# Optimization experiments

Hardware: AMD Instinct MI355X
Metric: run time of the kernel (lower is better)

## Reference

```python
import jax, jax.numpy as jnp
import numpy as np

GROUPS = 2048   # number of FPS centroids S
K = 24          # ball-query neighbors
RADIUS = 0.2    # ball radius (xyz in unit cube)


def setup_inputs() -> dict:
    key = jax.random.key(0)
    k1, k2 = jax.random.split(key)
    xyz = jax.random.uniform(k1, (8, 8192, 3), dtype=jnp.float32)
    points = jax.random.normal(k2, (8, 8192, 128), dtype=jnp.float32)
    return {"xyz": xyz, "points": points}


def _fps(xyz, npoint):
    # iterative farthest point sampling; deterministic start at index 0
    B, N, _ = xyz.shape

    def step(carry, _):
        distance, farthest = carry                       # [B,N], [B]
        centroid = jnp.take_along_axis(xyz, farthest[:, None, None], axis=1)  # [B,1,3]
        d = jnp.sum((xyz - centroid) ** 2, axis=-1)      # [B,N]
        distance = jnp.minimum(distance, d)
        nxt = jnp.argmax(distance, axis=-1).astype(jnp.int32)
        return (distance, nxt), farthest

    init = (jnp.full((B, N), 1e10, jnp.float32), jnp.zeros((B,), jnp.int32))
    _, idxs = jax.lax.scan(step, init, None, length=npoint)  # [npoint,B]
    return jnp.transpose(idxs)                               # [B,npoint]


def _index_points(points, idx):
    # points [B,N,C], idx [B,...] -> [B,...,C]
    B = idx.shape[0]
    flat = idx.reshape(B, -1)
    out = jnp.take_along_axis(points, flat[..., None], axis=1)
    return out.reshape(*idx.shape, points.shape[-1])


def _square_distance(src, dst):
    # src [B,N,C], dst [B,M,C] -> [B,N,M]
    return (jnp.sum(src ** 2, -1)[..., None]
            + jnp.sum(dst ** 2, -1)[:, None, :]
            - 2.0 * jnp.einsum('bnc,bmc->bnm', src, dst))


def _query_ball(radius, nsample, xyz, new_xyz):
    B, N, _ = xyz.shape
    sqr = _square_distance(new_xyz, xyz)                 # [B,S,N]
    base = jnp.arange(N, dtype=jnp.int32)
    idx = jnp.where(sqr > radius * radius, jnp.int32(N), base)  # out-of-ball -> N
    idx = jnp.sort(idx, axis=-1)[..., :nsample]          # [B,S,k]
    first = idx[..., :1]
    return jnp.where(idx == N, first, idx)


def reference(xyz, points):
    B, N, _ = xyz.shape
    fps_idx = _fps(xyz, GROUPS)                          # [B,S]
    new_xyz = _index_points(xyz, fps_idx)                # [B,S,3]
    anchor_feat = _index_points(points, fps_idx)         # [B,S,D]
    idx = _query_ball(RADIUS, K, xyz, new_xyz)           # [B,S,k]
    grouped_xyz = _index_points(xyz, idx)                # [B,S,k,3]
    grouped_points = _index_points(points, idx)          # [B,S,k,D]
    grouped = jnp.concatenate([grouped_points, grouped_xyz], axis=-1)  # use_xyz=True
    anchor = jnp.broadcast_to(anchor_feat[:, :, None, :],
                              (B, GROUPS, K, points.shape[-1]))
    new_points = jnp.concatenate([grouped, anchor], axis=-1)  # [B,S,k,2D+3]
    return new_xyz, new_points
```

## Files before the change

kernel.cpp:

```cpp
#include <hip/hip_runtime.h>
#include <stdint.h>


#define NBATCH 8
#define NPTS   8192
#define NCH    128
#define NGROUP 2048
#define NK     24
#define ROWLEN (2 * NCH + 3)

#define FPS_T  512
#define PPT    16

typedef float v2f __attribute__((ext_vector_type(2)));

struct __attribute__((packed, aligned(4))) f4s { float x, y, z, w; };

__device__ __forceinline__ float sq3_nofma(float dx, float dy, float dz) {
#pragma clang fp contract(off)
  return dx * dx + dy * dy + dz * dz;
}

__device__ __forceinline__ float dot3_fma(float ax, float ay, float az,
                                          float bx, float by, float bz) {
  float acc = __fmul_rn(ax, bx);
  acc = __fmaf_rn(ay, by, acc);
  acc = __fmaf_rn(az, bz, acc);
  return acc;
}

__device__ __forceinline__ float ballquery_sqr(float srcSq, float dstSq, float dot) {
#pragma clang fp contract(off)
  return (srcSq + dstSq) - 2.0f * dot;
}

template <int CTRL>
__device__ __forceinline__ float maxdpp(float v) {
  int s = __builtin_amdgcn_update_dpp(__builtin_bit_cast(int, v),
                                      __builtin_bit_cast(int, v),
                                      CTRL, 0xF, 0xF, false);
  return fmaxf(v, __builtin_bit_cast(float, s));
}

__device__ __forceinline__ float readlane_f(float v, int lane) {
  return __builtin_bit_cast(float,
      __builtin_amdgcn_readlane(__builtin_bit_cast(int, v), lane));
}

__global__ __launch_bounds__(FPS_T) void fps_kernel(const float* __restrict__ xyz,
                                                    int* __restrict__ fps_idx) {
  const int b = blockIdx.x;
  const int t = threadIdx.x;
  const int lane = t & 63;
  const int w = t >> 6;
  const float* xb = xyz + (size_t)b * NPTS * 3;

  __shared__ float s_xyz[NPTS * 3];
  union pair_t { struct { float v; int i; }; unsigned long long u; };
  __shared__ __align__(16) pair_t s_p[2][8];

  {
    const float4* src4 = (const float4*)xb;
    float4* dst4 = (float4*)s_xyz;
    for (int i = t; i < (NPTS * 3) / 4; i += FPS_T) dst4[i] = src4[i];
  }

  const int base = t * PPT;
  v2f px[8], py[8], pz[8], d2[8];
#pragma unroll
  for (int j = 0; j < 8; ++j) {
    const int n0 = base + 2 * j;
    px[j].x = xb[n0 * 3 + 0]; py[j].x = xb[n0 * 3 + 1]; pz[j].x = xb[n0 * 3 + 2];
    px[j].y = xb[n0 * 3 + 3]; py[j].y = xb[n0 * 3 + 4]; pz[j].y = xb[n0 * 3 + 5];
    d2[j].x = 1e10f; d2[j].y = 1e10f;
  }

  float cx = xb[0], cy = xb[1], cz = xb[2];
  if (t == 0) fps_idx[b * NGROUP + 0] = 0;

  for (int s = 1; s < NGROUP; ++s) {
    const int p = s & 1;

    float lv = -1.0f;
#pragma unroll
    for (int j = 0; j < 8; ++j) {
      v2f dx, dy, dz, dd, nd;
      {
#pragma clang fp contract(off)
        dx = px[j] - cx;
        dy = py[j] - cy;
        dz = pz[j] - cz;
        dd = dx * dx + dy * dy + dz * dz;
      }
      nd.x = fminf(d2[j].x, dd.x);
      nd.y = fminf(d2[j].y, dd.y);
      d2[j] = nd;
      lv = fmaxf(fmaxf(nd.x, nd.y), lv);
    }
    int kk = 0;
#pragma unroll
    for (int j = 7; j >= 0; --j) {
      if (d2[j].y == lv) kk = 2 * j + 1;
      if (d2[j].x == lv) kk = 2 * j;
    }
    const int li = base + kk;

    float v = lv;
    v = maxdpp<0x111>(v);
    v = maxdpp<0x112>(v);
    v = maxdpp<0x114>(v);
    v = maxdpp<0x118>(v);
    v = maxdpp<0x142>(v);
    v = maxdpp<0x143>(v);
    const float wmax = readlane_f(v, 63);
    const unsigned long long m = __ballot(lv == wmax);
    const int wl = (int)__builtin_ctzll(m);
    const int wli = __builtin_amdgcn_readlane(li, wl);
    if (lane == 0) {
      s_p[p][w].u = ((unsigned long long)(unsigned)wli << 32) |
                    (unsigned long long)__builtin_bit_cast(unsigned, wmax);
    }
    __syncthreads();

    const float4* q = (const float4*)&s_p[p][0];
    const float4 q0 = q[0], q1 = q[1], q2 = q[2], q3 = q[3];
    float bv = q0.x;
    float biF = q0.y;
    {
      const float vv[7] = { q0.z, q1.x, q1.z, q2.x, q2.z, q3.x, q3.z };
      const float ii[7] = { q0.w, q1.y, q1.w, q2.y, q2.w, q3.y, q3.w };
#pragma unroll
      for (int k = 0; k < 7; ++k) {
        const bool gt = vv[k] > bv;
        bv  = gt ? vv[k] : bv;
        biF = gt ? ii[k] : biF;
      }
    }
    const int bi = __builtin_bit_cast(int, biF);

    if (t == 0) fps_idx[b * NGROUP + s] = bi;

    const int b3 = bi * 3;
    cx = s_xyz[b3 + 0];
    cy = s_xyz[b3 + 1];
    cz = s_xyz[b3 + 2];
  }
}

__global__ __launch_bounds__(256) void group_kernel(const float* __restrict__ xyz,
                                                    const float* __restrict__ points,
                                                    const int* __restrict__ fps_idx,
                                                    float* __restrict__ out) {
  const int bx = blockIdx.x;
  const int gb = ((bx & 7) << 11) | (bx >> 3);
  const int b = gb >> 11;
  const int tid = threadIdx.x;
  const float* xb = xyz + (size_t)b * NPTS * 3;
  const float* pb = points + (size_t)b * NPTS * NCH;

  __shared__ int s_idx[NK];

  const int a_idx = fps_idx[gb];
  const float cx = xb[a_idx * 3 + 0];
  const float cy = xb[a_idx * 3 + 1];
  const float cz = xb[a_idx * 3 + 2];
  const float srcSq = sq3_nofma(cx, cy, cz);
  const float R2 = (float)(0.2 * 0.2);

  if (tid < 64) {
    int cnt = 0;
    int first = 0;
    const unsigned long long below = ((unsigned long long)1 << tid) - 1ull;
    for (int chunk = 0; chunk < NPTS / 128; ++chunk) {
      const int n0 = (chunk << 7) + (tid << 1);
      const float* p = xb + (size_t)n0 * 3;
      const float2 A = *(const float2*)(p + 0);
      const float2 Bv = *(const float2*)(p + 2);
      const float2 C = *(const float2*)(p + 4);
      const float x0 = A.x, y0 = A.y, z0 = Bv.x;
      const float x1 = Bv.y, y1 = C.x, z1 = C.y;

      const float sqr0 = ballquery_sqr(srcSq, sq3_nofma(x0, y0, z0),
                                       dot3_fma(cx, cy, cz, x0, y0, z0));
      const float sqr1 = ballquery_sqr(srcSq, sq3_nofma(x1, y1, z1),
                                       dot3_fma(cx, cy, cz, x1, y1, z1));
      const bool ok0 = !(sqr0 > R2);
      const bool ok1 = !(sqr1 > R2);
      const unsigned long long m0 = __ballot(ok0);
      const unsigned long long m1 = __ballot(ok1);
      if (cnt == 0 && (m0 | m1)) {
        const int f0 = m0 ? (int)__builtin_ctzll(m0) : 64;
        const int f1 = m1 ? (int)__builtin_ctzll(m1) : 64;
        first = (f0 <= f1) ? ((chunk << 7) + 2 * f0) : ((chunk << 7) + 2 * f1 + 1);
      }
      const int p0 = cnt + (int)__popcll(m0 & below) + (int)__popcll(m1 & below);
      const int p1 = p0 + (ok0 ? 1 : 0);
      if (ok0 && p0 < NK) s_idx[p0] = n0;
      if (ok1 && p1 < NK) s_idx[p1] = n0 + 1;
      cnt += (int)__popcll(m0) + (int)__popcll(m1);
      if (cnt >= NK) break;
    }
    if (tid >= cnt && tid < NK) s_idx[tid] = first;
  }
  __syncthreads();

  if (tid == 0) {
    float* onx = out + (size_t)gb * 3;
    onx[0] = cx; onx[1] = cy; onx[2] = cz;
  }

  float* op = out + (size_t)NBATCH * NGROUP * 3 + (size_t)gb * (NK * ROWLEN);
  const float* anchor = pb + (size_t)a_idx * NCH;

#pragma unroll
  for (int it = 0; it < 3; ++it) {
    const int vidx = tid + (it << 8);
    const int k = vidx >> 5;
    const int c4 = vidx & 31;
    const int si = s_idx[k];
    const f4s val = *(const f4s*)(pb + (size_t)si * NCH + (c4 << 2));
    *(f4s*)(op + k * ROWLEN + (c4 << 2)) = val;
  }
#pragma unroll
  for (int it = 0; it < 3; ++it) {
    const int vidx = tid + (it << 8);
    const int k = vidx >> 5;
    const int c4 = vidx & 31;
    const f4s val = *(const f4s*)(anchor + (c4 << 2));
    *(f4s*)(op + k * ROWLEN + (NCH + 3) + (c4 << 2)) = val;
  }
  if (tid < NK * 3) {
    const int k = tid / 3;
    const int r = tid - k * 3;
    const int si = s_idx[k];
    op[k * ROWLEN + NCH + r] = xb[si * 3 + r];
  }
}

extern "C" void kernel_launch(void* const* d_in, const int* in_sizes, int n_in,
                              void* d_out, int out_size, void* d_ws, size_t ws_size,
                              hipStream_t stream) {
  const float* xyz = (const float*)d_in[0];
  const float* points = (const float*)d_in[1];
  float* out = (float*)d_out;
  int* fps_idx = (int*)d_ws;

  fps_kernel<<<dim3(NBATCH), dim3(FPS_T), 0, stream>>>(xyz, fps_idx);
  group_kernel<<<dim3(NBATCH * NGROUP), dim3(256), 0, stream>>>(xyz, points, fps_idx, out);
}
```

Baseline: 2.134 ms.

## Fuse FPS and grouping into one persistent kernel with flag-based streaming

Merges the sequential FPS kernel and the grouping kernel into one launch. Eight blocks run FPS and publish each centroid index with atomic stores, while 248 persistent consumer blocks spin on a -1-initialised workspace and perform ball query and gather as soon as each index appears. The aim is to hide the grouping and gather work behind the long serial FPS loop. It adds a memset, spin-waiting, and a deadlock risk if the FPS blocks are not all co-resident with the consumers, and the consumer blocks may contend for resources with the FPS blocks.

```diff
diff --git a/kernel.cpp b/kernel.cpp
--- a/kernel.cpp
+++ b/kernel.cpp
@@ -9,8 +9,11 @@
 #define NK     24
 #define ROWLEN (2 * NCH + 3)
 
-#define FPS_T  512
-#define PPT    16
+#define FPS_T   512
+#define PPT     16
+#define GBLOCKS 248
+#define GSLOTS  62
+#define GITERS  34
 
 typedef float v2f __attribute__((ext_vector_type(2)));
 
@@ -47,193 +50,221 @@
       __builtin_amdgcn_readlane(__builtin_bit_cast(int, v), lane));
 }
 
-__global__ __launch_bounds__(FPS_T) void fps_kernel(const float* __restrict__ xyz,
-                                                    int* __restrict__ fps_idx) {
-  const int b = blockIdx.x;
+__global__ __launch_bounds__(FPS_T) void fused_kernel(const float* __restrict__ xyz,
+                                                      const float* __restrict__ points,
+                                                      int* __restrict__ fps_idx,
+                                                      float* __restrict__ out) {
   const int t = threadIdx.x;
-  const int lane = t & 63;
-  const int w = t >> 6;
-  const float* xb = xyz + (size_t)b * NPTS * 3;
 
   __shared__ float s_xyz[NPTS * 3];
   union pair_t { struct { float v; int i; }; unsigned long long u; };
   __shared__ __align__(16) pair_t s_p[2][8];
-
-  {
-    const float4* src4 = (const float4*)xb;
-    float4* dst4 = (float4*)s_xyz;
-    for (int i = t; i < (NPTS * 3) / 4; i += FPS_T) dst4[i] = src4[i];
+  __shared__ int s_aidx[2];
+  __shared__ int s_idx2[2][NK];
+
+  if (blockIdx.x < NBATCH) {
+    const int b = blockIdx.x;
+    const int lane = t & 63;
+    const int w = t >> 6;
+    const float* xb = xyz + (size_t)b * NPTS * 3;
+
+    {
+      const float4* src4 = (const float4*)xb;
+      float4* dst4 = (float4*)s_xyz;
+      for (int i = t; i < (NPTS * 3) / 4; i += FPS_T) dst4[i] = src4[i];
+    }
+
+    const int base = t * PPT;
+    v2f px[8], py[8], pz[8], d2[8];
+#pragma unroll
+    for (int j = 0; j < 8; ++j) {
+      const int n0 = base + 2 * j;
+      px[j].x = xb[n0 * 3 + 0]; py[j].x = xb[n0 * 3 + 1]; pz[j].x = xb[n0 * 3 + 2];
+      px[j].y = xb[n0 * 3 + 3]; py[j].y = xb[n0 * 3 + 4]; pz[j].y = xb[n0 * 3 + 5];
+      d2[j].x = 1e10f; d2[j].y = 1e10f;
+    }
+
+    float cx = xb[0], cy = xb[1], cz = xb[2];
+    if (t == 0)
+      __hip_atomic_store(&fps_idx[b * NGROUP + 0], 0,
+                         __ATOMIC_RELAXED, __HIP_MEMORY_SCOPE_AGENT);
+
+    for (int s = 1; s < NGROUP; ++s) {
+      const int p = s & 1;
+
+      float lv = -1.0f;
+#pragma unroll
+      for (int j = 0; j < 8; ++j) {
+        v2f dx, dy, dz, dd, nd;
+        {
+#pragma clang fp contract(off)
+          dx = px[j] - cx;
+          dy = py[j] - cy;
+          dz = pz[j] - cz;
+          dd = dx * dx + dy * dy + dz * dz;
+        }
+        nd.x = fminf(d2[j].x, dd.x);
+        nd.y = fminf(d2[j].y, dd.y);
+        d2[j] = nd;
+        lv = fmaxf(fmaxf(nd.x, nd.y), lv);
+      }
+      int kk = 0;
+#pragma unroll
+      for (int j = 7; j >= 0; --j) {
+        if (d2[j].y == lv) kk = 2 * j + 1;
+        if (d2[j].x == lv) kk = 2 * j;
+      }
+      const int li = base + kk;
+
+      float v = lv;
+      v = maxdpp<0x111>(v);
+      v = maxdpp<0x112>(v);
+      v = maxdpp<0x114>(v);
+      v = maxdpp<0x118>(v);
+      v = maxdpp<0x142>(v);
+      v = maxdpp<0x143>(v);
+      const float wmax = readlane_f(v, 63);
+      const unsigned long long m = __ballot(lv == wmax);
+      const int wl = (int)__builtin_ctzll(m);
+      const int wli = __builtin_amdgcn_readlane(li, wl);
+      if (lane == 0) {
+        s_p[p][w].u = ((unsigned long long)(unsigned)wli << 32) |
+                      (unsigned long long)__builtin_bit_cast(unsigned, wmax);
+      }
+      __syncthreads();
+
+      const float4* q = (const float4*)&s_p[p][0];
+      const float4 q0 = q[0], q1 = q[1], q2 = q[2], q3 = q[3];
+      float bv = q0.x;
+      float biF = q0.y;
+      {
+        const float vv[7] = { q0.z, q1.x, q1.z, q2.x, q2.z, q3.x, q3.z };
+        const float ii[7] = { q0.w, q1.y, q1.w, q2.y, q2.w, q3.y, q3.w };
+#pragma unroll
+        for (int k = 0; k < 7; ++k) {
+          const bool gt = vv[k] > bv;
+          bv  = gt ? vv[k] : bv;
+          biF = gt ? ii[k] : biF;
+        }
+      }
+      const int bi = __builtin_bit_cast(int, biF);
+
+      if (t == 0)
+        __hip_atomic_store(&fps_idx[b * NGROUP + s], bi,
+                           __ATOMIC_RELAXED, __HIP_MEMORY_SCOPE_AGENT);
+
+      const int b3 = bi * 3;
+      cx = s_xyz[b3 + 0];
+      cy = s_xyz[b3 + 1];
+      cz = s_xyz[b3 + 2];
+    }
+    return;
   }
 
-  const int base = t * PPT;
-  v2f px[8], py[8], pz[8], d2[8];
-#pragma unroll
-  for (int j = 0; j < 8; ++j) {
-    const int n0 = base + 2 * j;
-    px[j].x = xb[n0 * 3 + 0]; py[j].x = xb[n0 * 3 + 1]; pz[j].x = xb[n0 * 3 + 2];
-    px[j].y = xb[n0 * 3 + 3]; py[j].y = xb[n0 * 3 + 4]; pz[j].y = xb[n0 * 3 + 5];
-    d2[j].x = 1e10f; d2[j].y = 1e10f;
-  }
-
-  float cx = xb[0], cy = xb[1], cz = xb[2];
-  if (t == 0) fps_idx[b * NGROUP + 0] = 0;
-
-  for (int s = 1; s < NGROUP; ++s) {
-    const int p = s & 1;
-
-    float lv = -1.0f;
-#pragma unroll
-    for (int j = 0; j < 8; ++j) {
-      v2f dx, dy, dz, dd, nd;
-      {
-#pragma clang fp contract(off)
-        dx = px[j] - cx;
-        dy = py[j] - cy;
-        dz = pz[j] - cz;
-        dd = dx * dx + dy * dy + dz * dz;
-      }
-      nd.x = fminf(d2[j].x, dd.x);
-      nd.y = fminf(d2[j].y, dd.y);
-      d2[j] = nd;
-      lv = fmaxf(fmaxf(nd.x, nd.y), lv);
-    }
-    int kk = 0;
-#pragma unroll
-    for (int j = 7; j >= 0; --j) {
-      if (d2[j].y == lv) kk = 2 * j + 1;
-      if (d2[j].x == lv) kk = 2 * j;
-    }
-    const int li = base + kk;
-
-    float v = lv;
-    v = maxdpp<0x111>(v);
-    v = maxdpp<0x112>(v);
-    v = maxdpp<0x114>(v);
-    v = maxdpp<0x118>(v);
-    v = maxdpp<0x142>(v);
-    v = maxdpp<0x143>(v);
-    const float wmax = readlane_f(v, 63);
-    const unsigned long long m = __ballot(lv == wmax);
-    const int wl = (int)__builtin_ctzll(m);
-    const int wli = __builtin_amdgcn_readlane(li, wl);
-    if (lane == 0) {
-      s_p[p][w].u = ((unsigned long long)(unsigned)wli << 32) |
-                    (unsigned long long)__builtin_bit_cast(unsigned, wmax);
-    }
-    __syncthreads();
-
-    const float4* q = (const float4*)&s_p[p][0];
-    const float4 q0 = q[0], q1 = q[1], q2 = q[2], q3 = q[3];
-    float bv = q0.x;
-    float biF = q0.y;
-    {
-      const float vv[7] = { q0.z, q1.x, q1.z, q2.x, q2.z, q3.x, q3.z };
-      const float ii[7] = { q0.w, q1.y, q1.w, q2.y, q2.w, q3.y, q3.w };
-#pragma unroll
-      for (int k = 0; k < 7; ++k) {
-        const bool gt = vv[k] > bv;
-        bv  = gt ? vv[k] : bv;
-        biF = gt ? ii[k] : biF;
-      }
-    }
-    const int bi = __builtin_bit_cast(int, biF);
-
-    if (t == 0) fps_idx[b * NGROUP + s] = bi;
-
-    const int b3 = bi * 3;
-    cx = s_xyz[b3 + 0];
-    cy = s_xyz[b3 + 1];
-    cz = s_xyz[b3 + 2];
-  }
-}
-
-__global__ __launch_bounds__(256) void group_kernel(const float* __restrict__ xyz,
-                                                    const float* __restrict__ points,
-                                                    const int* __restrict__ fps_idx,
-                                                    float* __restrict__ out) {
-  const int bx = blockIdx.x;
-  const int gb = ((bx & 7) << 11) | (bx >> 3);
-  const int b = gb >> 11;
-  const int tid = threadIdx.x;
+  const int gs = blockIdx.x - NBATCH;
+  const int b = gs & 7;
+  const int sb = gs >> 3;
+  const int h = t >> 8;
+  const int htid = t & 255;
   const float* xb = xyz + (size_t)b * NPTS * 3;
   const float* pb = points + (size_t)b * NPTS * NCH;
-
-  __shared__ int s_idx[NK];
-
-  const int a_idx = fps_idx[gb];
-  const float cx = xb[a_idx * 3 + 0];
-  const float cy = xb[a_idx * 3 + 1];
-  const float cz = xb[a_idx * 3 + 2];
-  const float srcSq = sq3_nofma(cx, cy, cz);
   const float R2 = (float)(0.2 * 0.2);
 
-  if (tid < 64) {
-    int cnt = 0;
-    int first = 0;
-    const unsigned long long below = ((unsigned long long)1 << tid) - 1ull;
-    for (int chunk = 0; chunk < NPTS / 128; ++chunk) {
-      const int n0 = (chunk << 7) + (tid << 1);
-      const float* p = xb + (size_t)n0 * 3;
-      const float2 A = *(const float2*)(p + 0);
-      const float2 Bv = *(const float2*)(p + 2);
-      const float2 C = *(const float2*)(p + 4);
-      const float x0 = A.x, y0 = A.y, z0 = Bv.x;
-      const float x1 = Bv.y, y1 = C.x, z1 = C.y;
-
-      const float sqr0 = ballquery_sqr(srcSq, sq3_nofma(x0, y0, z0),
-                                       dot3_fma(cx, cy, cz, x0, y0, z0));
-      const float sqr1 = ballquery_sqr(srcSq, sq3_nofma(x1, y1, z1),
-                                       dot3_fma(cx, cy, cz, x1, y1, z1));
-      const bool ok0 = !(sqr0 > R2);
-      const bool ok1 = !(sqr1 > R2);
-      const unsigned long long m0 = __ballot(ok0);
-      const unsigned long long m1 = __ballot(ok1);
-      if (cnt == 0 && (m0 | m1)) {
-        const int f0 = m0 ? (int)__builtin_ctzll(m0) : 64;
-        const int f1 = m1 ? (int)__builtin_ctzll(m1) : 64;
-        first = (f0 <= f1) ? ((chunk << 7) + 2 * f0) : ((chunk << 7) + 2 * f1 + 1);
-      }
-      const int p0 = cnt + (int)__popcll(m0 & below) + (int)__popcll(m1 & below);
-      const int p1 = p0 + (ok0 ? 1 : 0);
-      if (ok0 && p0 < NK) s_idx[p0] = n0;
-      if (ok1 && p1 < NK) s_idx[p1] = n0 + 1;
-      cnt += (int)__popcll(m0) + (int)__popcll(m1);
-      if (cnt >= NK) break;
-    }
-    if (tid >= cnt && tid < NK) s_idx[tid] = first;
-  }
-  __syncthreads();
-
-  if (tid == 0) {
-    float* onx = out + (size_t)gb * 3;
-    onx[0] = cx; onx[1] = cy; onx[2] = cz;
-  }
-
-  float* op = out + (size_t)NBATCH * NGROUP * 3 + (size_t)gb * (NK * ROWLEN);
-  const float* anchor = pb + (size_t)a_idx * NCH;
-
-#pragma unroll
-  for (int it = 0; it < 3; ++it) {
-    const int vidx = tid + (it << 8);
-    const int k = vidx >> 5;
-    const int c4 = vidx & 31;
-    const int si = s_idx[k];
-    const f4s val = *(const f4s*)(pb + (size_t)si * NCH + (c4 << 2));
-    *(f4s*)(op + k * ROWLEN + (c4 << 2)) = val;
-  }
-#pragma unroll
-  for (int it = 0; it < 3; ++it) {
-    const int vidx = tid + (it << 8);
-    const int k = vidx >> 5;
-    const int c4 = vidx & 31;
-    const f4s val = *(const f4s*)(anchor + (c4 << 2));
-    *(f4s*)(op + k * ROWLEN + (NCH + 3) + (c4 << 2)) = val;
-  }
-  if (tid < NK * 3) {
-    const int k = tid / 3;
-    const int r = tid - k * 3;
-    const int si = s_idx[k];
-    op[k * ROWLEN + NCH + r] = xb[si * 3 + r];
+  for (int i = 0; i < GITERS; ++i) {
+    const int g = i * GSLOTS + sb * 2 + h;
+    const bool act = g < NGROUP;
+    const int gb = (b << 11) | (g & 2047);
+
+    if (htid == 0 && act) {
+      int v;
+      while ((v = __hip_atomic_load(&fps_idx[gb], __ATOMIC_RELAXED,
+                                    __HIP_MEMORY_SCOPE_AGENT)) == -1)
+        __builtin_amdgcn_s_sleep(8);
+      s_aidx[h] = v;
+    }
+    __syncthreads();
+
+    int a_idx = 0;
+    float cx = 0.f, cy = 0.f, cz = 0.f, srcSq = 0.f;
+    if (act) {
+      a_idx = s_aidx[h];
+      cx = xb[a_idx * 3 + 0];
+      cy = xb[a_idx * 3 + 1];
+      cz = xb[a_idx * 3 + 2];
+      srcSq = sq3_nofma(cx, cy, cz);
+
+      if (htid < 64) {
+        int cnt = 0;
+        int first = 0;
+        const unsigned long long below = ((unsigned long long)1 << htid) - 1ull;
+        for (int chunk = 0; chunk < NPTS / 128; ++chunk) {
+          const int n0 = (chunk << 7) + (htid << 1);
+          const float* p = xb + (size_t)n0 * 3;
+          const float2 A = *(const float2*)(p + 0);
+          const float2 Bv = *(const float2*)(p + 2);
+          const float2 C = *(const float2*)(p + 4);
+          const float x0 = A.x, y0 = A.y, z0 = Bv.x;
+          const float x1 = Bv.y, y1 = C.x, z1 = C.y;
+
+          const float sqr0 = ballquery_sqr(srcSq, sq3_nofma(x0, y0, z0),
+                                           dot3_fma(cx, cy, cz, x0, y0, z0));
+          const float sqr1 = ballquery_sqr(srcSq, sq3_nofma(x1, y1, z1),
+                                           dot3_fma(cx, cy, cz, x1, y1, z1));
+          const bool ok0 = !(sqr0 > R2);
+          const bool ok1 = !(sqr1 > R2);
+          const unsigned long long m0 = __ballot(ok0);
+          const unsigned long long m1 = __ballot(ok1);
+          if (cnt == 0 && (m0 | m1)) {
+            const int f0 = m0 ? (int)__builtin_ctzll(m0) : 64;
+            const int f1 = m1 ? (int)__builtin_ctzll(m1) : 64;
+            first = (f0 <= f1) ? ((chunk << 7) + 2 * f0) : ((chunk << 7) + 2 * f1 + 1);
+          }
+          const int p0 = cnt + (int)__popcll(m0 & below) + (int)__popcll(m1 & below);
+          const int p1 = p0 + (ok0 ? 1 : 0);
+          if (ok0 && p0 < NK) s_idx2[h][p0] = n0;
+          if (ok1 && p1 < NK) s_idx2[h][p1] = n0 + 1;
+          cnt += (int)__popcll(m0) + (int)__popcll(m1);
+          if (cnt >= NK) break;
+        }
+        if (htid >= cnt && htid < NK) s_idx2[h][htid] = first;
+      }
+    }
+    __syncthreads();
+
+    if (act) {
+      if (htid == 0) {
+        float* onx = out + (size_t)gb * 3;
+        onx[0] = cx; onx[1] = cy; onx[2] = cz;
+      }
+
+      float* op = out + (size_t)NBATCH * NGROUP * 3 + (size_t)gb * (NK * ROWLEN);
+      const float* anchor = pb + (size_t)a_idx * NCH;
+
+#pragma unroll
+      for (int it = 0; it < 3; ++it) {
+        const int vidx = htid + (it << 8);
+        const int k = vidx >> 5;
+        const int c4 = vidx & 31;
+        const int si = s_idx2[h][k];
+        const f4s val = *(const f4s*)(pb + (size_t)si * NCH + (c4 << 2));
+        *(f4s*)(op + k * ROWLEN + (c4 << 2)) = val;
+      }
+#pragma unroll
+      for (int it = 0; it < 3; ++it) {
+        const int vidx = htid + (it << 8);
+        const int k = vidx >> 5;
+        const int c4 = vidx & 31;
+        const f4s val = *(const f4s*)(anchor + (c4 << 2));
+        *(f4s*)(op + k * ROWLEN + (NCH + 3) + (c4 << 2)) = val;
+      }
+      if (htid < NK * 3) {
+        const int k = htid / 3;
+        const int r = htid - k * 3;
+        const int si = s_idx2[h][k];
+        op[k * ROWLEN + NCH + r] = xb[si * 3 + r];
+      }
+    }
+    __syncthreads();
   }
 }
 
@@ -245,6 +276,6 @@
   float* out = (float*)d_out;
   int* fps_idx = (int*)d_ws;
 
-  fps_kernel<<<dim3(NBATCH), dim3(FPS_T), 0, stream>>>(xyz, fps_idx);
-  group_kernel<<<dim3(NBATCH * NGROUP), dim3(256), 0, stream>>>(xyz, points, fps_idx, out);
-}
+  hipMemsetAsync(d_ws, 0xFF, (size_t)NBATCH * NGROUP * sizeof(int), stream);
+  fused_kernel<<<dim3(NBATCH + GBLOCKS), dim3(FPS_T), 0, stream>>>(xyz, points, fps_idx, out);
+}
```

Measured after the change: 2.034 ms. 1.05x faster.
